# Kernel tuning notes

Measured on AMD Instinct MI355X. Metric: run time of the kernel, lower is better.

The kernel has to match this reference:

```python
import jax, jax.numpy as jnp
import numpy as np

EPS = 1e-6  # torch.nn.PairwiseDistance default eps (added to the difference)


def setup_inputs() -> dict:
    key = jax.random.key(0)
    k1, k2 = jax.random.split(key)
    support = jax.random.normal(k1, (25, 2560), dtype=jnp.float32)
    query = jax.random.normal(k2, (4096, 2560), dtype=jnp.float32)
    return {"support": support, "query": query, "n_way": 5, "k_shot": 5}


def reference(support, query, n_way, k_shot):
    # support: [n_way*k_shot, cdd], query: [qsize, cdd]
    qsize = query.shape[0]
    support = support.reshape(support.shape[0], -1)
    query = query.reshape(qsize, -1)
    # pairwise L2 distance with torch PairwiseDistance semantics: ||x1 - x2 + eps||_2
    diff = support[None, :, :] - query[:, None, :] + EPS  # [qsize, n_way*k_shot, cdd]
    dist = jnp.sqrt(jnp.sum(diff * diff, axis=-1))        # [qsize, n_way*k_shot]
    score = -dist.reshape(qsize, n_way, k_shot).sum(axis=2)  # [qsize, n_way]
    return score
```

## Files before the change

### kernel.cpp

```cpp
#include <hip/hip_runtime.h>
#include <hip/hip_bf16.h>
#include <math.h>


#define EPS 1e-6f
#define D 2560
#define NSUP 25
#define NQ 4096
#define NWAY 5
#define KSHOT 5

#define QR 4
#define BT 128
#define KITER 10
#define NSL 13
#define NACC 60
#define STRIDE 61

__global__ void prep_kernel(const float* __restrict__ sup, float* __restrict__ ns) {
    const int s = blockIdx.x;
    const int t = threadIdx.x;
    float p = 0.f;
    #pragma unroll
    for (int k = 0; k < 10; ++k) {
        float v = sup[s * D + t + 256 * k] + EPS;
        p += v * v;
    }
    __shared__ float red[256];
    red[t] = p;
    __syncthreads();
    for (int off = 128; off > 0; off >>= 1) {
        if (t < off) red[t] += red[t + off];
        __syncthreads();
    }
    if (t == 0) ns[s] = red[0];
}

__global__ __launch_bounds__(BT, 2)
void pairwise_kernel(const float* __restrict__ q, const float* __restrict__ sup,
                     const float* __restrict__ ns, float* __restrict__ out) {
    const int t = threadIdx.x;
    const int lane = t & 63;
    const int wave = t >> 6;
    const int row0 = blockIdx.x * QR;
    const int sup_base = wave * (NSL - 1);

    float acc[NACC];
    #pragma unroll
    for (int i = 0; i < NACC; ++i) acc[i] = 0.f;

    #pragma unroll 1
    for (int k = 0; k < KITER; ++k) {
        const int idx = 4 * lane + 256 * k;
        float4 q4[QR];
        #pragma unroll
        for (int r = 0; r < QR; ++r)
            q4[r] = *reinterpret_cast<const float4*>(&q[(row0 + r) * D + idx]);
        #pragma unroll
        for (int r = 0; r < QR; ++r) {
            acc[52 + r] += (q4[r].x + q4[r].y) + (q4[r].z + q4[r].w);
            acc[56 + r] += q4[r].x * q4[r].x + q4[r].y * q4[r].y
                         + q4[r].z * q4[r].z + q4[r].w * q4[r].w;
        }
        #pragma unroll
        for (int g = 0; g < NSL; g += 4) {
            const int ge = (g + 4 < NSL) ? g + 4 : NSL;
            float4 a4[4];
            #pragma unroll
            for (int j = g; j < ge; ++j)
                a4[j - g] = *reinterpret_cast<const float4*>(&sup[(sup_base + j) * D + idx]);
            #pragma unroll
            for (int j = g; j < ge; ++j) {
                #pragma unroll
                for (int r = 0; r < QR; ++r) {
                    acc[r * NSL + j] += a4[j - g].x * q4[r].x + a4[j - g].y * q4[r].y
                                      + a4[j - g].z * q4[r].z + a4[j - g].w * q4[r].w;
                }
            }
        }
    }

    __shared__ float buf[BT * STRIDE];
    __shared__ float red0[NACC];
    __shared__ float red1[NACC];
    __shared__ float dist[100];

    #pragma unroll
    for (int v = 0; v < NACC; ++v) buf[t * STRIDE + v] = acc[v];
    __syncthreads();

    if (lane < NACC) {
        const int base = wave * 64;
        float s0 = 0.f, s1 = 0.f, s2 = 0.f, s3 = 0.f;
        for (int i = 0; i < 64; i += 4) {
            s0 += buf[(base + i + 0) * STRIDE + lane];
            s1 += buf[(base + i + 1) * STRIDE + lane];
            s2 += buf[(base + i + 2) * STRIDE + lane];
            s3 += buf[(base + i + 3) * STRIDE + lane];
        }
        const float tot = (s0 + s1) + (s2 + s3);
        if (wave == 0) red0[lane] = tot;
        else           red1[lane] = tot;
    }
    __syncthreads();

    if (t < 100) {
        const int r = t / NSUP, s = t % NSUP;
        const float dot = (s < NSL) ? red0[r * NSL + s] : red1[r * NSL + (s - (NSL - 1))];
        const float d2 = ns[s] + red0[56 + r] - 2.f * (dot + EPS * red0[52 + r]);
        dist[t] = sqrtf(fmaxf(d2, 0.f));
    }
    __syncthreads();
    if (t < QR * NWAY) {
        const int r = t / NWAY, w = t % NWAY;
        float sc = 0.f;
        #pragma unroll
        for (int j = 0; j < KSHOT; ++j) sc += dist[r * NSUP + w * KSHOT + j];
        out[(row0 + r) * NWAY + w] = -sc;
    }
}

extern "C" void kernel_launch(void* const* d_in, const int* in_sizes, int n_in,
                              void* d_out, int out_size, void* d_ws, size_t ws_size,
                              hipStream_t stream) {
    const float* support = (const float*)d_in[0];
    const float* query   = (const float*)d_in[1];
    float* out = (float*)d_out;
    float* ns  = (float*)d_ws;

    prep_kernel<<<NSUP, 256, 0, stream>>>(support, ns);
    pairwise_kernel<<<NQ / QR, BT, 0, stream>>>(query, support, ns, out);
}
```

Baseline: 96.49 us.

## Split feature dimension across two wave pairs and reduce accumulators in two phases

Doubles the block to 256 threads. Each pair of waves now splits the 2560-wide feature dimension in half, so each thread runs 5 loop iterations instead of 10. The cross-thread reduction is done in two phases of 30 accumulators, which keeps the shared buffer the same size despite twice as many threads. The aim is more wave-level parallelism and occupancy, at the cost of an extra barrier round and a longer reduction per lane.

```diff
diff --git a/kernel.cpp b/kernel.cpp
--- a/kernel.cpp
+++ b/kernel.cpp
@@ -11,11 +11,12 @@
 #define KSHOT 5
 
 #define QR 4
-#define BT 128
-#define KITER 10
+#define BT 256
+#define KITER 5
 #define NSL 13
 #define NACC 60
-#define STRIDE 61
+#define PH 30
+#define STRIDE 31
 
 __global__ void prep_kernel(const float* __restrict__ sup, float* __restrict__ ns) {
     const int s = blockIdx.x;
@@ -36,22 +37,24 @@
     if (t == 0) ns[s] = red[0];
 }
 
-__global__ __launch_bounds__(BT, 2)
+__global__ __launch_bounds__(BT, 4)
 void pairwise_kernel(const float* __restrict__ q, const float* __restrict__ sup,
                      const float* __restrict__ ns, float* __restrict__ out) {
     const int t = threadIdx.x;
     const int lane = t & 63;
     const int wave = t >> 6;
+    const int sg = wave >> 1;
+    const int dg = wave & 1;
     const int row0 = blockIdx.x * QR;
-    const int sup_base = wave * (NSL - 1);
+    const int sup_base = sg * (NSL - 1);
 
     float acc[NACC];
     #pragma unroll
     for (int i = 0; i < NACC; ++i) acc[i] = 0.f;
 
     #pragma unroll 1
-    for (int k = 0; k < KITER; ++k) {
-        const int idx = 4 * lane + 256 * k;
+    for (int j = 0; j < KITER; ++j) {
+        const int idx = 4 * lane + 512 * j + 256 * dg;
         float4 q4[QR];
         #pragma unroll
         for (int r = 0; r < QR; ++r)
@@ -67,14 +70,14 @@
             const int ge = (g + 4 < NSL) ? g + 4 : NSL;
             float4 a4[4];
             #pragma unroll
-            for (int j = g; j < ge; ++j)
-                a4[j - g] = *reinterpret_cast<const float4*>(&sup[(sup_base + j) * D + idx]);
+            for (int jj = g; jj < ge; ++jj)
+                a4[jj - g] = *reinterpret_cast<const float4*>(&sup[(sup_base + jj) * D + idx]);
             #pragma unroll
-            for (int j = g; j < ge; ++j) {
+            for (int jj = g; jj < ge; ++jj) {
                 #pragma unroll
                 for (int r = 0; r < QR; ++r) {
-                    acc[r * NSL + j] += a4[j - g].x * q4[r].x + a4[j - g].y * q4[r].y
-                                      + a4[j - g].z * q4[r].z + a4[j - g].w * q4[r].w;
+                    acc[r * NSL + jj] += a4[jj - g].x * q4[r].x + a4[jj - g].y * q4[r].y
+                                       + a4[jj - g].z * q4[r].z + a4[jj - g].w * q4[r].w;
                 }
             }
         }
@@ -85,24 +88,26 @@
     __shared__ float red1[NACC];
     __shared__ float dist[100];
 
-    #pragma unroll
-    for (int v = 0; v < NACC; ++v) buf[t * STRIDE + v] = acc[v];
-    __syncthreads();
-
-    if (lane < NACC) {
-        const int base = wave * 64;
-        float s0 = 0.f, s1 = 0.f, s2 = 0.f, s3 = 0.f;
-        for (int i = 0; i < 64; i += 4) {
-            s0 += buf[(base + i + 0) * STRIDE + lane];
-            s1 += buf[(base + i + 1) * STRIDE + lane];
-            s2 += buf[(base + i + 2) * STRIDE + lane];
-            s3 += buf[(base + i + 3) * STRIDE + lane];
+    #pragma unroll 1
+    for (int p = 0; p < 2; ++p) {
+        #pragma unroll
+        for (int v = 0; v < PH; ++v) buf[t * STRIDE + v] = acc[p * PH + v];
+        __syncthreads();
+        if ((wave == 0 || wave == 2) && lane < PH) {
+            const int base = (wave >> 1) * 128;
+            float s0 = 0.f, s1 = 0.f, s2 = 0.f, s3 = 0.f;
+            for (int i = 0; i < 128; i += 4) {
+                s0 += buf[(base + i + 0) * STRIDE + lane];
+                s1 += buf[(base + i + 1) * STRIDE + lane];
+                s2 += buf[(base + i + 2) * STRIDE + lane];
+                s3 += buf[(base + i + 3) * STRIDE + lane];
+            }
+            const float tot = (s0 + s1) + (s2 + s3);
+            if (wave == 0) red0[p * PH + lane] = tot;
+            else           red1[p * PH + lane] = tot;
         }
-        const float tot = (s0 + s1) + (s2 + s3);
-        if (wave == 0) red0[lane] = tot;
-        else           red1[lane] = tot;
+        __syncthreads();
     }
-    __syncthreads();
 
     if (t < 100) {
         const int r = t / NSUP, s = t % NSUP;
```

New measurement: 291.6 us. 3.02x slower.
